# Performance work log

Measured on AMD Instinct MI355X. Metric: run time of the kernel, lower is better.

Reference implementation:

```python
import jax, jax.numpy as jnp
import numpy as np

T, B, D, R, H = 16, 1024, 1024, 8, 16
DH = D // H


def setup_inputs() -> dict:
    key = jax.random.key(0)
    ks = jax.random.split(key, 10)
    s = 1.0 / np.sqrt(D)
    return {
        "table_embs": jax.random.normal(ks[0], (T, B, D), jnp.float32),
        "rel_embs": jax.random.normal(ks[1], (T, R, D), jnp.float32),
        "rel_idx": jax.random.randint(ks[2], (T, R), 0, T),
        "Wq": jax.random.normal(ks[3], (D, D), jnp.float32) * s,
        "bq": jnp.zeros((D,), jnp.float32),
        "Wk": jax.random.normal(ks[4], (D, D), jnp.float32) * s,
        "bk": jnp.zeros((D,), jnp.float32),
        "Wv": jax.random.normal(ks[5], (D, D), jnp.float32) * s,
        "bv": jnp.zeros((D,), jnp.float32),
        "Wo": jax.random.normal(ks[6], (D, D), jnp.float32) * s,
        "bo": jnp.zeros((D,), jnp.float32),
        "w_rel": jax.random.normal(ks[7], (D,), jnp.float32) * s,
        "b_rel": jnp.zeros((1,), jnp.float32),
    }


def reference(table_embs, rel_embs, rel_idx, Wq, bq, Wk, bk, Wv, bv, Wo, bo, w_rel, b_rel):
    # relationship weights: sigmoid(Linear(rel_emb)) -> scalar per (table, relation)
    rel_w = jax.nn.sigmoid(rel_embs @ w_rel + b_rel[0])          # [T, R]
    # gather related tables' embeddings and apply relationship weight
    others = table_embs[rel_idx]                                  # [T, R, B, D]
    weighted = others * rel_w[:, :, None, None]                   # [T, R, B, D]
    kv_src = jnp.transpose(weighted, (0, 2, 1, 3))                # [T, B, R, D]
    # MultiheadAttention, q_len=1, kv_len=R (PyTorch convention: x @ W.T + b)
    q = (table_embs @ Wq.T + bq).reshape(T, B, H, DH)             # [T, B, H, DH]
    k = (kv_src @ Wk.T + bk).reshape(T, B, R, H, DH)              # [T, B, R, H, DH]
    v = (kv_src @ Wv.T + bv).reshape(T, B, R, H, DH)
    scores = jnp.einsum("tbhd,tbrhd->tbhr", q, k) / np.sqrt(DH)   # [T, B, H, R]
    attn = jax.nn.softmax(scores, axis=-1)
    ctx = jnp.einsum("tbhr,tbrhd->tbhd", attn, v).reshape(T, B, D)
    return ctx @ Wo.T + bo                                        # [T, B, D]
```

## Files before the change

### kernel.cpp

```cpp
#include <hip/hip_runtime.h>


typedef unsigned short u16;
typedef __attribute__((ext_vector_type(8))) short short8;
typedef __attribute__((ext_vector_type(4))) float f32x4;

__device__ __forceinline__ float bf2f(u16 u) {
  unsigned int x = ((unsigned int)u) << 16;
  return __uint_as_float(x);
}
__device__ __forceinline__ u16 f2bf(float f) {
  unsigned int x = __float_as_uint(f);
  unsigned int r = (x + 0x7fffu + ((x >> 16) & 1u)) >> 16;
  return (u16)r;
}

__device__ __forceinline__ void gld_lds16(const void* g, void* l) {
  __builtin_amdgcn_global_load_lds(
      (const __attribute__((address_space(1))) unsigned int*)(unsigned long long)g,
      (__attribute__((address_space(3))) unsigned int*)(unsigned int)(unsigned long long)l,
      16, 0, 0);
}

#define VWAIT(N) asm volatile("s_waitcnt vmcnt(" #N ")" ::: "memory")


__global__ void relw_kernel(const float* __restrict__ rel_embs,
                            const float* __restrict__ w_rel,
                            const float* __restrict__ b_rel,
                            float* __restrict__ rel_w) {
  const int tr = blockIdx.x;
  const float* row = rel_embs + (size_t)tr * 1024;
  const int lane = threadIdx.x;
  float s = 0.f;
  for (int i = lane; i < 1024; i += 64) s += row[i] * w_rel[i];
  for (int off = 32; off > 0; off >>= 1) s += __shfl_down(s, off, 64);
  if (lane == 0) rel_w[tr] = 1.f / (1.f + __expf(-(s + b_rel[0])));
}

__global__ void cvt_f32_bf16(const float* __restrict__ in, u16* __restrict__ out, int n4) {
  int i = blockIdx.x * blockDim.x + threadIdx.x;
  if (i >= n4) return;
  float4 v = ((const float4*)in)[i];
  ushort4 o;
  o.x = f2bf(v.x); o.y = f2bf(v.y); o.z = f2bf(v.z); o.w = f2bf(v.w);
  ((ushort4*)out)[i] = o;
}

__global__ void cvt_w4(const float* __restrict__ Wq, const float* __restrict__ Wk,
                       const float* __restrict__ Wv, const float* __restrict__ Wo,
                       u16* __restrict__ Wcat, u16* __restrict__ Wob) {
  const int i = blockIdx.x * 256 + threadIdx.x;
  const int w = i >> 18;
  const int j = i & 0x3ffff;
  const float* src = (w == 0) ? Wq : (w == 1) ? Wk : (w == 2) ? Wv : Wo;
  u16* dst = (w == 3) ? Wob : (Wcat + ((size_t)w << 20));
  float4 v = ((const float4*)src)[j];
  ushort4 o;
  o.x = f2bf(v.x); o.y = f2bf(v.y); o.z = f2bf(v.z); o.w = f2bf(v.w);
  ((ushort4*)dst)[j] = o;
}


__device__ __forceinline__ void mainloop256(const u16* __restrict__ A,
                                            const u16* __restrict__ B,
                                            u16* lds, int m0, int n0,
                                            f32x4 (&acc)[8][4]) {
  const int tid  = threadIdx.x;
  const int lane = tid & 63;
  const int w    = tid >> 6;
  const int wm   = w >> 2, wn = w & 3;
  const int fr   = lane & 15, fq = lane >> 4;
  const int swz  = fr & 7;

  const unsigned A0 = 0, B0 = 16384, A1 = 32768, B1 = 49152;

  const int srow = tid >> 3;
  const int lc   = (tid & 7) ^ (srow & 7);
  const u16* a0p = A + (size_t)(m0 + srow) * 1024 + lc * 8;
  const u16* b0p = B + (size_t)(n0 + srow) * 1024 + lc * 8;
  const unsigned d0 = (unsigned)((tid & ~63) * 8);

  const u16 *ap0[2], *ap1[2], *bp0[2], *bp1[2];
#pragma unroll
  for (int ks = 0; ks < 2; ++ks) {
    const unsigned ck = (unsigned)((((ks << 2) + fq) ^ swz) << 3);
    ap0[ks] = lds + A0 + (wm * 128 + fr) * 64 + ck;
    ap1[ks] = lds + A1 + (wm * 128 + fr) * 64 + ck;
    bp0[ks] = lds + B0 + (wn * 64 + fr) * 64 + ck;
    bp1[ks] = lds + B1 + (wn * 64 + fr) * 64 + ck;
  }

#define STAGE_B4(BO)                                                           \
  do {                                                                         \
    gld_lds16(b0p + 0 * 65536, lds + (BO) + d0 + 0 * 4096);                    \
    gld_lds16(b0p + 1 * 65536, lds + (BO) + d0 + 1 * 4096);                    \
    gld_lds16(b0p + 2 * 65536, lds + (BO) + d0 + 2 * 4096);                    \
    gld_lds16(b0p + 3 * 65536, lds + (BO) + d0 + 3 * 4096);                    \
    b0p += 64;                                                                 \
  } while (0)

#define STAGE_A2(ra, rb, AO)                                                   \
  do {                                                                         \
    gld_lds16(a0p + (ra) * 65536, lds + (AO) + d0 + (ra) * 4096);              \
    gld_lds16(a0p + (rb) * 65536, lds + (AO) + d0 + (rb) * 4096);              \
  } while (0)

#define PHASE_Q(q, ap, STMT)                                                   \
  do {                                                                         \
    short8 a0k0 = *(const short8*)((ap)[0] + (2*(q))   * 1024);                \
    short8 a1k0 = *(const short8*)((ap)[0] + (2*(q)+1) * 1024);                \
    short8 a0k1 = *(const short8*)((ap)[1] + (2*(q))   * 1024);                \
    short8 a1k1 = *(const short8*)((ap)[1] + (2*(q)+1) * 1024);                \
    STMT;                                                                      \
    __builtin_amdgcn_s_barrier();                                              \
    __builtin_amdgcn_s_setprio(1);                                             \
    _Pragma("unroll")                                                          \
    for (int j = 0; j < 4; ++j) {                                              \
      acc[2*(q)][j]   = __builtin_amdgcn_mfma_f32_16x16x32_bf16(a0k0, bgv[j][0], acc[2*(q)][j],   0, 0, 0); \
      acc[2*(q)+1][j] = __builtin_amdgcn_mfma_f32_16x16x32_bf16(a1k0, bgv[j][0], acc[2*(q)+1][j], 0, 0, 0); \
    }                                                                          \
    _Pragma("unroll")                                                          \
    for (int j = 0; j < 4; ++j) {                                              \
      acc[2*(q)][j]   = __builtin_amdgcn_mfma_f32_16x16x32_bf16(a0k1, bgv[j][1], acc[2*(q)][j],   0, 0, 0); \
      acc[2*(q)+1][j] = __builtin_amdgcn_mfma_f32_16x16x32_bf16(a1k1, bgv[j][1], acc[2*(q)+1][j], 0, 0, 0); \
    }                                                                          \
    __builtin_amdgcn_s_setprio(0);                                             \
  } while (0)

#define BGV_LOAD(bp)                                                           \
  _Pragma("unroll")                                                            \
  for (int j = 0; j < 4; ++j) {                                                \
    bgv[j][0] = *(const short8*)((bp)[0] + j * 1024);                          \
    bgv[j][1] = *(const short8*)((bp)[1] + j * 1024);                          \
  }

#define KTILE(ap, bp, AO_N, BO_N)                                              \
  do {                                                                         \
    short8 bgv[4][2];                                                          \
    BGV_LOAD(bp);                                                              \
    PHASE_Q(0, ap, { STAGE_B4(BO_N); });                                       \
    __builtin_amdgcn_s_barrier();                                              \
    PHASE_Q(1, ap, { STAGE_A2(0, 2, AO_N); });                                 \
    VWAIT(6);                                                                  \
    __builtin_amdgcn_s_barrier();                                              \
    PHASE_Q(2, ap, { STAGE_A2(1, 3, AO_N); a0p += 64; });                      \
    __builtin_amdgcn_s_barrier();                                              \
    PHASE_Q(3, ap, {});                                                       \
    VWAIT(2);                                                                  \
    __builtin_amdgcn_s_barrier();                                              \
  } while (0)

#define KTILE_LAST(ap, bp)                                                     \
  do {                                                                         \
    short8 bgv[4][2];                                                          \
    BGV_LOAD(bp);                                                              \
    PHASE_Q(0, ap, {});                                                       \
    __builtin_amdgcn_s_barrier();                                              \
    PHASE_Q(1, ap, {});                                                       \
    VWAIT(0);                                                                  \
    __builtin_amdgcn_s_barrier();                                              \
    PHASE_Q(2, ap, {});                                                       \
    __builtin_amdgcn_s_barrier();                                              \
    PHASE_Q(3, ap, {});                                                       \
    __builtin_amdgcn_s_barrier();                                              \
  } while (0)

  gld_lds16(b0p + 0 * 65536, lds + B0 + d0 + 0 * 4096);
  gld_lds16(b0p + 1 * 65536, lds + B0 + d0 + 1 * 4096);
  gld_lds16(b0p + 2 * 65536, lds + B0 + d0 + 2 * 4096);
  gld_lds16(b0p + 3 * 65536, lds + B0 + d0 + 3 * 4096);
  gld_lds16(a0p + 0 * 65536, lds + A0 + d0 + 0 * 4096);
  gld_lds16(a0p + 2 * 65536, lds + A0 + d0 + 2 * 4096);
  gld_lds16(a0p + 1 * 65536, lds + A0 + d0 + 1 * 4096);
  gld_lds16(a0p + 3 * 65536, lds + A0 + d0 + 3 * 4096);
  a0p += 64; b0p += 64;
  VWAIT(2);
  __builtin_amdgcn_s_barrier();

  for (int it = 0; it < 7; ++it) {
    KTILE(ap0, bp0, A1, B1);
    KTILE(ap1, bp1, A0, B0);
  }
  KTILE(ap0, bp0, A1, B1);
  KTILE_LAST(ap1, bp1);

#undef STAGE_B4
#undef STAGE_A2
#undef PHASE_Q
#undef BGV_LOAD
#undef KTILE
#undef KTILE_LAST
}

__device__ __forceinline__ void xcd_swizzle(int nx, int ny, int& bx, int& by) {
  const int nwg = nx * ny;
  int bid = by * nx + bx;
  bid = (bid & 7) * (nwg >> 3) + (bid >> 3);
  bx = bid % nx;
  by = bid / nx;
}

__global__ __launch_bounds__(512, 1)
void gemm_qkv(const u16* __restrict__ A, const u16* __restrict__ Bw,
              const float* __restrict__ bq,
              u16* __restrict__ Qt, u16* __restrict__ Kt, u16* __restrict__ Vt) {
  __shared__ __align__(16) u16 lds[65536];
  int bx = blockIdx.x, by = blockIdx.y;
  xcd_swizzle(gridDim.x, gridDim.y, bx, by);
  const int n0 = bx * 256;
  const int m0 = by * 256;
  f32x4 acc[8][4];
#pragma unroll
  for (int i = 0; i < 8; ++i)
#pragma unroll
    for (int j = 0; j < 4; ++j) acc[i][j] = (f32x4){0.f, 0.f, 0.f, 0.f};

  mainloop256(A, Bw, lds, m0, n0, acc);
  __syncthreads();

  const int tid  = threadIdx.x;
  const int lane = tid & 63;
  const int w    = tid >> 6;
  const int wm   = w >> 2, wn = w & 3;
  const int colw = lane & 15, roww = (lane >> 4) * 4;
  const int t = m0 >> 10, b0 = m0 & 1023;
  const int sel = n0 >> 10, dbase = n0 & 1023;
  u16* outp = (sel == 0) ? Qt : (sel == 1) ? Kt : Vt;

  {
    char* reg = (char*)(lds + wm * 32768);
#pragma unroll
    for (int j = 0; j < 4; ++j) {
      const int dl = wn * 64 + j * 16 + colw;
      const float badd = (sel == 0) ? bq[dbase + dl] : 0.f;
      char* rowp = reg + (unsigned)dl * 256;
      const unsigned sx = ((unsigned)dl & 7) << 4;
#pragma unroll
      for (int i = 0; i < 8; ++i) {
        const int bl = i * 16 + roww;
        uint2 pv;
        pv.x = (unsigned)f2bf(acc[i][j][0] + badd)
             | ((unsigned)f2bf(acc[i][j][1] + badd) << 16);
        pv.y = (unsigned)f2bf(acc[i][j][2] + badd)
             | ((unsigned)f2bf(acc[i][j][3] + badd) << 16);
        *(uint2*)(rowp + (((unsigned)bl * 2) ^ sx)) = pv;
      }
    }
  }
  __syncthreads();
#pragma unroll
  for (int pass = 0; pass < 2; ++pass) {
    const char* regp = (const char*)(lds + pass * 32768);
#pragma unroll
    for (int rr = 0; rr < 8; ++rr) {
      const int slot = rr * 512 + tid;
      const int row = slot >> 4, c16 = slot & 15;
      const uint4 v = *(const uint4*)(regp + (unsigned)row * 256
                                      + (((unsigned)c16 * 16) ^ (((unsigned)row & 7) << 4)));
      *(uint4*)(outp + ((size_t)t << 20) + (size_t)(dbase + row) * 1024
                + b0 + pass * 128 + c16 * 8) = v;
    }
  }
}

__global__ __launch_bounds__(512, 1)
void gemm_out(const u16* __restrict__ A, const u16* __restrict__ Bw,
              const float* __restrict__ bo, float* __restrict__ out) {
  __shared__ __align__(16) u16 lds[65536];
  int bx = blockIdx.x, by = blockIdx.y;
  xcd_swizzle(gridDim.x, gridDim.y, bx, by);
  const int n0 = bx * 256;
  const int m0 = by * 256;
  f32x4 acc[8][4];
#pragma unroll
  for (int i = 0; i < 8; ++i)
#pragma unroll
    for (int j = 0; j < 4; ++j) acc[i][j] = (f32x4){0.f, 0.f, 0.f, 0.f};

  mainloop256(A, Bw, lds, m0, n0, acc);

  const int lane = threadIdx.x & 63;
  const int w    = threadIdx.x >> 6;
  const int wm   = w >> 2, wn = w & 3;
  const int colw = lane & 15, roww = (lane >> 4) * 4;
#pragma unroll
  for (int j = 0; j < 4; ++j) {
    const int gn = n0 + wn * 64 + j * 16 + colw;
    const float bov = bo[gn];
#pragma unroll
    for (int i = 0; i < 8; ++i) {
      const int gm = m0 + wm * 128 + i * 16 + roww;
#pragma unroll
      for (int r = 0; r < 4; ++r)
        out[(size_t)(gm + r) * 1024 + gn] = acc[i][j][r] + bov;
    }
  }
}

__global__ __launch_bounds__(256)
void attn5(const u16* __restrict__ Qt, const u16* __restrict__ Kt,
           const u16* __restrict__ Vt,
           const float* __restrict__ relw, const int* __restrict__ rel_idx,
           const float* __restrict__ bk, const float* __restrict__ bv,
           u16* __restrict__ ctx) {
  const int tid = threadIdx.x;
  const int h = blockIdx.y, t = blockIdx.z;
  const int b0 = blockIdx.x * 256;
  const int b = b0 + tid;
  const int hd = h * 64;

  __shared__ u16  st[256 * 34];
  __shared__ float bks[64], bvs[64], rws[8];
  __shared__ int   rids[8];

  if (tid < 64) { bks[tid] = bk[hd + tid]; bvs[tid] = bv[hd + tid]; }
  else if (tid < 72) { rws[tid - 64] = relw[t * 8 + (tid - 64)];
                       rids[tid - 64] = rel_idx[t * 8 + (tid - 64)]; }
  __syncthreads();

  const unsigned qoff = ((unsigned)t << 20) + ((unsigned)hd << 10) + (unsigned)b;
  unsigned koff[8];
#pragma unroll
  for (int r = 0; r < 8; ++r)
    koff[r] = ((unsigned)rids[r] << 20) + ((unsigned)hd << 10) + (unsigned)b;

  float acc[8];
#pragma unroll
  for (int r = 0; r < 8; ++r) acc[r] = 0.f;
  float qbk = 0.f;
#pragma unroll 4
  for (int d = 0; d < 64; ++d) {
    const float q = bf2f(Qt[qoff + d * 1024]);
    qbk += q * bks[d];
#pragma unroll
    for (int r = 0; r < 8; ++r)
      acc[r] += q * bf2f(Kt[koff[r] + d * 1024]);
  }

  float w[8];
  {
    float s[8], mx = -1e30f;
#pragma unroll
    for (int r = 0; r < 8; ++r) {
      s[r] = (rws[r] * acc[r] + qbk) * 0.125f;
      mx = fmaxf(mx, s[r]);
    }
    float sum = 0.f;
#pragma unroll
    for (int r = 0; r < 8; ++r) { s[r] = __expf(s[r] - mx); sum += s[r]; }
    const float inv = 1.f / sum;
#pragma unroll
    for (int r = 0; r < 8; ++r) w[r] = s[r] * inv * rws[r];
  }

  for (int half = 0; half < 2; ++half) {
#pragma unroll
    for (int dp = 0; dp < 32; dp += 2) {
      const int d = half * 32 + dp;
      float o0 = bvs[d];
      float o1 = bvs[d + 1];
#pragma unroll
      for (int r = 0; r < 8; ++r) {
        o0 += w[r] * bf2f(Vt[koff[r] + d * 1024]);
        o1 += w[r] * bf2f(Vt[koff[r] + (d + 1) * 1024]);
      }
      const unsigned p = (unsigned)f2bf(o0) | ((unsigned)f2bf(o1) << 16);
      *(unsigned*)(st + tid * 34 + dp) = p;
    }
    __syncthreads();
    {
      const int sub = tid & 7;
      const int rbase = tid >> 3;
#pragma unroll
      for (int p = 0; p < 8; ++p) {
        const int row = p * 32 + rbase;
        const uint2 v = *(const uint2*)(st + row * 34 + sub * 4);
        *(uint2*)(ctx + ((size_t)(t * 1024 + b0 + row)) * 1024
                  + hd + half * 32 + sub * 4) = v;
      }
    }
    __syncthreads();
  }
}


extern "C" void kernel_launch(void* const* d_in, const int* in_sizes, int n_in,
                              void* d_out, int out_size, void* d_ws, size_t ws_size,
                              hipStream_t stream) {
  const float* table = (const float*)d_in[0];
  const float* rele  = (const float*)d_in[1];
  const int*   ridx  = (const int*)d_in[2];
  const float* Wq    = (const float*)d_in[3];
  const float* bq    = (const float*)d_in[4];
  const float* Wk    = (const float*)d_in[5];
  const float* bk    = (const float*)d_in[6];
  const float* Wv    = (const float*)d_in[7];
  const float* bv    = (const float*)d_in[8];
  const float* Wo    = (const float*)d_in[9];
  const float* bo    = (const float*)d_in[10];
  const float* wr    = (const float*)d_in[11];
  const float* br    = (const float*)d_in[12];
  float* out = (float*)d_out;

  char* ws = (char*)d_ws;
  const size_t MB = 1024 * 1024;
  u16*  Xbf  = (u16*)(ws);
  u16*  Kt   = (u16*)(ws + 32  * MB);
  u16*  Vt   = (u16*)(ws + 64  * MB);
  u16*  Qt   = (u16*)(ws + 96  * MB);
  u16*  Wcat = (u16*)(ws + 128 * MB);
  u16*  Wob  = (u16*)(ws + 134 * MB);
  float* relw = (float*)(ws + 136 * MB);
  u16*  ctxb = Xbf;

  relw_kernel<<<128, 64, 0, stream>>>(rele, wr, br, relw);
  cvt_f32_bf16<<<16384, 256, 0, stream>>>(table, Xbf, 4194304);
  cvt_w4<<<4096, 256, 0, stream>>>(Wq, Wk, Wv, Wo, Wcat, Wob);

  gemm_qkv<<<dim3(12, 64), 512, 0, stream>>>(Xbf, Wcat, bq, Qt, Kt, Vt);
  attn5<<<dim3(4, 16, 16), 256, 0, stream>>>(Qt, Kt, Vt, relw, ridx, bk, bv, ctxb);
  gemm_out<<<dim3(4, 64), 512, 0, stream>>>(ctxb, Wob, bo, out);
}
```

Baseline: 359.8 us.

## Software-pipeline LDS fragment reads one phase ahead of MFMA in GEMM mainloop

Restructures the GEMM k-loop so the A fragments for the next quarter-phase, and the B fragments for the next k-tile, are read from LDS while the current phase's MFMAs run. It uses double-buffered register fragments (afA/afB, bfr[2]) and rearranges the barriers and vmcnt waits. The goal is to hide LDS read latency behind matrix-core work and drop one barrier per phase. The cost is higher VGPR pressure and a fragile barrier/wait ordering that has to keep the LDS buffers safe from being overwritten early.

```diff
diff --git a/kernel.cpp b/kernel.cpp
--- a/kernel.cpp
+++ b/kernel.cpp
@@ -91,6 +91,8 @@
     bp1[ks] = lds + B1 + (wn * 64 + fr) * 64 + ck;
   }
 
+  short8 afA[4], afB[4], bfr[2][8];
+
 #define STAGE_B4(BO)                                                           \
   do {                                                                         \
     gld_lds16(b0p + 0 * 65536, lds + (BO) + d0 + 0 * 4096);                    \
@@ -106,64 +108,76 @@
     gld_lds16(a0p + (rb) * 65536, lds + (AO) + d0 + (rb) * 4096);              \
   } while (0)
 
-#define PHASE_Q(q, ap, STMT)                                                   \
-  do {                                                                         \
-    short8 a0k0 = *(const short8*)((ap)[0] + (2*(q))   * 1024);                \
-    short8 a1k0 = *(const short8*)((ap)[0] + (2*(q)+1) * 1024);                \
-    short8 a0k1 = *(const short8*)((ap)[1] + (2*(q))   * 1024);                \
-    short8 a1k1 = *(const short8*)((ap)[1] + (2*(q)+1) * 1024);                \
-    STMT;                                                                      \
-    __builtin_amdgcn_s_barrier();                                              \
+#define RD_A(dst, ap, q)                                                       \
+  do {                                                                         \
+    dst[0] = *(const short8*)((ap)[0] + (2*(q))   * 1024);                     \
+    dst[1] = *(const short8*)((ap)[0] + (2*(q)+1) * 1024);                     \
+    dst[2] = *(const short8*)((ap)[1] + (2*(q))   * 1024);                     \
+    dst[3] = *(const short8*)((ap)[1] + (2*(q)+1) * 1024);                     \
+  } while (0)
+
+#define RD_B(TB, bp)                                                           \
+  _Pragma("unroll")                                                            \
+  for (int j = 0; j < 4; ++j) {                                                \
+    bfr[TB][2*j]   = *(const short8*)((bp)[0] + j * 1024);                     \
+    bfr[TB][2*j+1] = *(const short8*)((bp)[1] + j * 1024);                     \
+  }
+
+#define MFMA_PH(q, S, TB)                                                      \
+  do {                                                                         \
     __builtin_amdgcn_s_setprio(1);                                             \
     _Pragma("unroll")                                                          \
     for (int j = 0; j < 4; ++j) {                                              \
-      acc[2*(q)][j]   = __builtin_amdgcn_mfma_f32_16x16x32_bf16(a0k0, bgv[j][0], acc[2*(q)][j],   0, 0, 0); \
-      acc[2*(q)+1][j] = __builtin_amdgcn_mfma_f32_16x16x32_bf16(a1k0, bgv[j][0], acc[2*(q)+1][j], 0, 0, 0); \
+      acc[2*(q)][j]   = __builtin_amdgcn_mfma_f32_16x16x32_bf16(S[0], bfr[TB][2*j], acc[2*(q)][j],   0, 0, 0); \
+      acc[2*(q)+1][j] = __builtin_amdgcn_mfma_f32_16x16x32_bf16(S[1], bfr[TB][2*j], acc[2*(q)+1][j], 0, 0, 0); \
     }                                                                          \
     _Pragma("unroll")                                                          \
     for (int j = 0; j < 4; ++j) {                                              \
-      acc[2*(q)][j]   = __builtin_amdgcn_mfma_f32_16x16x32_bf16(a0k1, bgv[j][1], acc[2*(q)][j],   0, 0, 0); \
-      acc[2*(q)+1][j] = __builtin_amdgcn_mfma_f32_16x16x32_bf16(a1k1, bgv[j][1], acc[2*(q)+1][j], 0, 0, 0); \
+      acc[2*(q)][j]   = __builtin_amdgcn_mfma_f32_16x16x32_bf16(S[2], bfr[TB][2*j+1], acc[2*(q)][j],   0, 0, 0); \
+      acc[2*(q)+1][j] = __builtin_amdgcn_mfma_f32_16x16x32_bf16(S[3], bfr[TB][2*j+1], acc[2*(q)+1][j], 0, 0, 0); \
     }                                                                          \
     __builtin_amdgcn_s_setprio(0);                                             \
   } while (0)
 
-#define BGV_LOAD(bp)                                                           \
-  _Pragma("unroll")                                                            \
-  for (int j = 0; j < 4; ++j) {                                                \
-    bgv[j][0] = *(const short8*)((bp)[0] + j * 1024);                          \
-    bgv[j][1] = *(const short8*)((bp)[1] + j * 1024);                          \
-  }
-
-#define KTILE(ap, bp, AO_N, BO_N)                                              \
-  do {                                                                         \
-    short8 bgv[4][2];                                                          \
-    BGV_LOAD(bp);                                                              \
-    PHASE_Q(0, ap, { STAGE_B4(BO_N); });                                       \
-    __builtin_amdgcn_s_barrier();                                              \
-    PHASE_Q(1, ap, { STAGE_A2(0, 2, AO_N); });                                 \
-    VWAIT(6);                                                                  \
-    __builtin_amdgcn_s_barrier();                                              \
-    PHASE_Q(2, ap, { STAGE_A2(1, 3, AO_N); a0p += 64; });                      \
-    __builtin_amdgcn_s_barrier();                                              \
-    PHASE_Q(3, ap, {});                                                       \
-    VWAIT(2);                                                                  \
-    __builtin_amdgcn_s_barrier();                                              \
-  } while (0)
-
-#define KTILE_LAST(ap, bp)                                                     \
-  do {                                                                         \
-    short8 bgv[4][2];                                                          \
-    BGV_LOAD(bp);                                                              \
-    PHASE_Q(0, ap, {});                                                       \
-    __builtin_amdgcn_s_barrier();                                              \
-    PHASE_Q(1, ap, {});                                                       \
+#define KTILE(apC, apN, bpN, TBC, TBN, AO_N, BO_N)                             \
+  do {                                                                         \
+                               \
+    RD_A(afB, apC, 1);                                                         \
+    STAGE_B4(BO_N);                                                            \
+    MFMA_PH(0, afA, TBC);                                                      \
+    VWAIT(4);                                         \
+    __builtin_amdgcn_s_barrier();                                              \
+                                          \
+    RD_A(afA, apC, 2);                                                         \
+    STAGE_A2(0, 2, AO_N);                                                      \
+    MFMA_PH(1, afB, TBC);                                                      \
+    __builtin_amdgcn_s_barrier();                                              \
+                                          \
+    RD_A(afB, apC, 3);                                                         \
+    STAGE_A2(1, 3, AO_N); a0p += 64;                                           \
+    MFMA_PH(2, afA, TBC);                                                      \
+    VWAIT(2);                                      \
+    __builtin_amdgcn_s_barrier();                                              \
+                         \
+    RD_A(afA, apN, 0);                                                         \
+    RD_B(TBN, bpN);                                                            \
+    MFMA_PH(3, afB, TBC);                                                      \
+    __builtin_amdgcn_s_barrier();                                              \
+  } while (0)
+
+#define KTILE_LAST(apC, TBC)                                                   \
+  do {                                                                         \
+    RD_A(afB, apC, 1);                                                         \
+    MFMA_PH(0, afA, TBC);                                                      \
     VWAIT(0);                                                                  \
     __builtin_amdgcn_s_barrier();                                              \
-    PHASE_Q(2, ap, {});                                                       \
-    __builtin_amdgcn_s_barrier();                                              \
-    PHASE_Q(3, ap, {});                                                       \
-    __builtin_amdgcn_s_barrier();                                              \
+    RD_A(afA, apC, 2);                                                         \
+    MFMA_PH(1, afB, TBC);                                                      \
+    __builtin_amdgcn_s_barrier();                                              \
+    RD_A(afB, apC, 3);                                                         \
+    MFMA_PH(2, afA, TBC);                                                      \
+    __builtin_amdgcn_s_barrier();                                              \
+    MFMA_PH(3, afB, TBC);                                                      \
   } while (0)
 
   gld_lds16(b0p + 0 * 65536, lds + B0 + d0 + 0 * 4096);
@@ -177,18 +191,21 @@
   a0p += 64; b0p += 64;
   VWAIT(2);
   __builtin_amdgcn_s_barrier();
+  RD_B(0, bp0);
+  RD_A(afA, ap0, 0);
 
   for (int it = 0; it < 7; ++it) {
-    KTILE(ap0, bp0, A1, B1);
-    KTILE(ap1, bp1, A0, B0);
-  }
-  KTILE(ap0, bp0, A1, B1);
-  KTILE_LAST(ap1, bp1);
+    KTILE(ap0, ap1, bp1, 0, 1, A1, B1);
+    KTILE(ap1, ap0, bp0, 1, 0, A0, B0);
+  }
+  KTILE(ap0, ap1, bp1, 0, 1, A1, B1);
+  KTILE_LAST(ap1, 1);
 
 #undef STAGE_B4
 #undef STAGE_A2
-#undef PHASE_Q
-#undef BGV_LOAD
+#undef RD_A
+#undef RD_B
+#undef MFMA_PH
 #undef KTILE
 #undef KTILE_LAST
 }
```

Result: slower. 368.8 us (+2.5%).
